# Kernel optimization log

Hardware: AMD Instinct MI355X
Metric: run time of the kernel (lower is better)

## Reference

```python
import jax, jax.numpy as jnp
import numpy as np


def _lstm_encode(x_tbF, W_ih, W_hh, b_ih, b_hh):
    """torch nn.LSTM (single layer), x: [T, B, F]. Returns final (h, c), each [B, H]."""
    H = W_hh.shape[1]
    B = x_tbF.shape[1]
    b = b_ih + b_hh

    def step(carry, xt):
        h, c = carry
        gates = xt @ W_ih.T + h @ W_hh.T + b  # [B, 4H]
        i, f, g, o = jnp.split(gates, 4, axis=-1)
        c = jax.nn.sigmoid(f) * c + jax.nn.sigmoid(i) * jnp.tanh(g)
        h = jax.nn.sigmoid(o) * jnp.tanh(c)
        return (h, c), None

    init = (jnp.zeros((B, H), x_tbF.dtype), jnp.zeros((B, H), x_tbF.dtype))
    (h, c), _ = jax.lax.scan(step, init, x_tbF)
    return h, c


def reference(speed, pos, Ws_ih, Ws_hh, bs_ih, bs_hh, Wp_ih, Wp_hh, bp_ih, bp_hh,
              Wd_ih, Wd_hh, bd_ih, bd_hh, W_fc, b_fc, W_emb, b_emb, seq_len):
    # Encoders consume time-major inputs (module does speed.permute(1,0,2))
    sh, sc = _lstm_encode(jnp.transpose(speed, (1, 0, 2)), Ws_ih, Ws_hh, bs_ih, bs_hh)
    ph, pc = _lstm_encode(jnp.transpose(pos, (1, 0, 2)), Wp_ih, Wp_hh, bp_ih, bp_hh)

    h0 = ph + sh
    c0 = pc + sc
    last_pos0 = pos[:, -1, :]  # [B, 4]
    bd = bd_ih + bd_hh

    def dec_step(carry, _):
        h, c, last_pos = carry
        gates = last_pos @ Wd_ih.T + h @ Wd_hh.T + bd  # [B, 4H]
        i, f, g, o = jnp.split(gates, 4, axis=-1)
        c = jax.nn.sigmoid(f) * c + jax.nn.sigmoid(i) * jnp.tanh(g)
        h = jax.nn.sigmoid(o) * jnp.tanh(c)
        crossing = jax.nn.relu(h @ W_fc.T + b_fc)        # fc_crossing: [B, 2]
        last_pos = jax.nn.relu(crossing @ W_emb.T + b_emb)  # pos_embedding: [B, 4]
        probs = jax.nn.softmax(crossing, axis=1)
        return (h, c, last_pos), probs

    _, probs = jax.lax.scan(dec_step, (h0, c0, last_pos0), None, length=seq_len)
    return jnp.transpose(probs, (1, 0, 2))  # [B, seq_len, 2]


def setup_inputs() -> dict:
    B, T, H, F = 8192, 16, 512, 4
    seq_len = 16
    key = jax.random.key(0)
    ks = jax.random.split(key, 20)
    s = 1.0 / np.sqrt(H)

    def u(k, shape):
        return jax.random.uniform(k, shape, jnp.float32, -s, s)

    return {
        "speed": jax.random.normal(ks[0], (B, T, F), jnp.float32),
        "pos": jax.random.normal(ks[1], (B, T, F), jnp.float32),
        "Ws_ih": u(ks[2], (4 * H, F)), "Ws_hh": u(ks[3], (4 * H, H)),
        "bs_ih": u(ks[4], (4 * H,)), "bs_hh": u(ks[5], (4 * H,)),
        "Wp_ih": u(ks[6], (4 * H, F)), "Wp_hh": u(ks[7], (4 * H, H)),
        "bp_ih": u(ks[8], (4 * H,)), "bp_hh": u(ks[9], (4 * H,)),
        "Wd_ih": u(ks[10], (4 * H, F)), "Wd_hh": u(ks[11], (4 * H, H)),
        "bd_ih": u(ks[12], (4 * H,)), "bd_hh": u(ks[13], (4 * H,)),
        "W_fc": u(ks[14], (2, H)), "b_fc": u(ks[15], (2,)),
        "W_emb": u(ks[16], (4, 2)), "b_emb": u(ks[17], (4,)),
        "seq_len": seq_len,
    }
```

## Files before the change

### kernel.cpp

```cpp
#include <hip/hip_runtime.h>

#define NBLK 256
#define NTHR 512
#define MTILE 32
#define KPADI 592
#define HSTR  528
#define CHB   (9*8*64*16)
#define LSTR  (16*CHB)

typedef __attribute__((ext_vector_type(4))) int int4v;

__device__ inline float ex2(float x){ return __builtin_amdgcn_exp2f(x); }
__device__ inline float rcpf_(float d){ return __builtin_amdgcn_rcpf(d); }
__device__ inline float rcpn(float d){ float r=__builtin_amdgcn_rcpf(d); return r*(2.f-d*r); }
#define LOG2E 1.4426950408889634f
__device__ inline float sigf(float x){ return rcpf_(1.f+ex2(-LOG2E*x)); }
__device__ inline float tanh_(float x){ return 2.f*rcpf_(1.f+ex2(-2.f*LOG2E*x))-1.f; }

__global__ void scale_k(const float* Ws_ih, const float* Ws_hh, const float* bs_ih, const float* bs_hh,
                        const float* Wp_ih, const float* Wp_hh, const float* bp_ih, const float* bp_hh,
                        const float* Wd_ih, const float* Wd_hh, const float* bd_ih, const float* bd_hh,
                        int* smax)
{
    int L = blockIdx.x >> 5;
    int blk = blockIdx.x & 31;
    const float* Wih = L==0 ? Ws_ih : L==1 ? Wp_ih : Wd_ih;
    const float* Whh = L==0 ? Ws_hh : L==1 ? Wp_hh : Wd_hh;
    const float* bih = L==0 ? bs_ih : L==1 ? bp_ih : bd_ih;
    const float* bhh = L==0 ? bs_hh : L==1 ? bp_hh : bd_hh;
    float m = 0.f;
    for (int i = blk*256 + threadIdx.x; i < 2048*512; i += 32*256) m = fmaxf(m, fabsf(Whh[i]));
    for (int i = blk*256 + threadIdx.x; i < 2048*4;   i += 32*256) m = fmaxf(m, fabsf(Wih[i]));
    for (int i = blk*256 + threadIdx.x; i < 2048;     i += 32*256) m = fmaxf(m, 0.5f*fabsf(bih[i]+bhh[i]));
    __shared__ float red[256];
    red[threadIdx.x] = m; __syncthreads();
    for (int s = 128; s; s >>= 1){
        if (threadIdx.x < s) red[threadIdx.x] = fmaxf(red[threadIdx.x], red[threadIdx.x+s]);
        __syncthreads();
    }
    if (threadIdx.x == 0) atomicMax(&smax[L], __float_as_int(red[0]));
}

__global__ void pack_k(const float* Wih, const float* Whh, const float* bih, const float* bhh,
                       const int* smax, int L, unsigned char* dst, float* gsout)
{
    int f4 = blockIdx.x*256 + threadIdx.x;
    if (f4*4 >= LSTR) return;
    float mx = __int_as_float(smax[L]);
    float inv = 127.f / mx;
    if (blockIdx.x==0 && threadIdx.x==0) gsout[L] = mx * (1.f/(127.f*127.f));
    int fb = f4*4;
    int lane=(fb>>4)&63, nt=(fb>>10)&7, t=fb>>13;
    int kt=t%9, chunk=t/9;
    int n = (chunk*8+nt)*16 + (lane&15);
    int ch=n>>7, g=(n>>5)&3, u=n&31;
    int row = g*512 + ch*32 + u;
    int kbase = kt*64 + ((lane>>4)<<4) + (fb&15);
    unsigned out = 0;
    #pragma unroll
    for (int b=0;b<4;++b){
        int k = kbase + b;
        float v = 0.f;
        if (k < 512)      v = Whh[row*512+k];
        else if (k < 528) v = Wih[row*4 + (k&3)];
        else if (k < 530) v = 0.5f*(bih[row]+bhh[row]);
        int q = (int)rintf(v*inv);
        q = q>127?127:(q<-127?-127:q);
        out |= ((unsigned)(q & 255)) << (8*b);
    }
    *(unsigned*)(dst + fb) = out;
}

__global__ __launch_bounds__(NTHR, 1)
void lstm_all(const float* __restrict__ speed, const float* __restrict__ pos,
              const unsigned char* __restrict__ wpack, const float* __restrict__ gsb,
              const float* __restrict__ wfc, const float* __restrict__ bfc,
              const float* __restrict__ wemb, const float* __restrict__ bemb,
              float* __restrict__ out)
{
    __shared__ __align__(16) unsigned char abuf[2][MTILE][KPADI];
    __shared__ __align__(16) unsigned char hsave[MTILE][HSTR];
    __shared__ float csave[MTILE][512];
    __shared__ float smallw[1040];
    __shared__ float partial[NTHR];

    const int tid  = threadIdx.x;
    const int lane = tid & 63;
    const int wv   = tid >> 6;
    const int row0 = blockIdx.x * MTILE;
    const int l15  = lane & 15;
    const int lq   = lane >> 4;
    const int cstag = blockIdx.x & 15;

    const float gs0 = gsb[0], gs1 = gsb[1], gs2 = gsb[2];

    {
        for (int i = tid; i < 2*MTILE*(KPADI/16); i += NTHR) {
            int b = i / (MTILE*(KPADI/16));
            int rmd = i % (MTILE*(KPADI/16));
            int m = rmd / (KPADI/16), c16 = (rmd % (KPADI/16))*16;
            *(int4v*)&abuf[b][m][c16] = (int4v){0,0,0,0};
        }
        for (int i = tid; i < 1024; i += NTHR) smallw[i] = wfc[i];
        if (tid < 2) smallw[1024+tid] = bfc[tid];
        if (tid < 8) smallw[1026+tid] = wemb[tid];
        if (tid < 4) smallw[1034+tid] = bemb[tid];
    }
    __syncthreads();
    if (tid < 64) { int b = tid>>5, m = tid&31; abuf[b][m][528] = 127; abuf[b][m][529] = 127; }
    if (tid < 128) {
        int m = tid>>2, f3 = tid&3;
        float x = speed[((size_t)(row0+m)*16 + 0)*4 + f3];
        int q = (int)rintf(fminf(fmaxf(x*31.75f,-127.f),127.f));
        unsigned char qb = (unsigned char)q;
        abuf[0][m][512+f3]=qb; abuf[0][m][516+f3]=qb; abuf[0][m][520+f3]=qb; abuf[0][m][524+f3]=qb;
    }
    __syncthreads();

    float cc0[16], cc1[16];
    #pragma unroll
    for (int i = 0; i < 16; ++i) { cc0[i]=0.f; cc1[i]=0.f; }

    auto pass = [&](int rb, int wbuf, const unsigned char* wl, int s, float (&cc)[16],
                    float gs, int DUAL, int DEFER, int (&hq)[16]) {
        const int chunk = (2*wv + s + cstag) & 15;
        const unsigned char* bp = wl + (size_t)chunk*CHB + lane*16;
        const unsigned char* ar0 = &abuf[rb][l15][0];
        const unsigned char* ar1 = &abuf[rb][16+l15][0];
        int4v acc[2][8];
        #pragma unroll
        for (int mf=0;mf<2;++mf)
            #pragma unroll
            for (int nt=0;nt<8;++nt) acc[mf][nt] = (int4v){0,0,0,0};
        int4v bA[8], bB[8];
        #pragma unroll
        for (int nt=0;nt<8;++nt) bA[nt] = *(const int4v*)(bp + nt*1024);
        #pragma unroll 1
        for (int kt=0; kt<8; kt+=2){
            const unsigned char* p1 = bp + (kt+1)*8192;
            #pragma unroll
            for (int nt=0;nt<8;++nt) bB[nt] = *(const int4v*)(p1 + nt*1024);
            int4v a0 = *(const int4v*)(ar0 + kt*64 + lq*16);
            int4v a1 = *(const int4v*)(ar1 + kt*64 + lq*16);
            #pragma unroll
            for (int nt=0;nt<8;++nt){
                acc[0][nt] = __builtin_amdgcn_mfma_i32_16x16x64_i8(a0, bA[nt], acc[0][nt], 0,0,0);
                acc[1][nt] = __builtin_amdgcn_mfma_i32_16x16x64_i8(a1, bA[nt], acc[1][nt], 0,0,0);
            }
            const unsigned char* p2 = bp + (kt+2)*8192;
            #pragma unroll
            for (int nt=0;nt<8;++nt) bA[nt] = *(const int4v*)(p2 + nt*1024);
            a0 = *(const int4v*)(ar0 + (kt+1)*64 + lq*16);
            a1 = *(const int4v*)(ar1 + (kt+1)*64 + lq*16);
            #pragma unroll
            for (int nt=0;nt<8;++nt){
                acc[0][nt] = __builtin_amdgcn_mfma_i32_16x16x64_i8(a0, bB[nt], acc[0][nt], 0,0,0);
                acc[1][nt] = __builtin_amdgcn_mfma_i32_16x16x64_i8(a1, bB[nt], acc[1][nt], 0,0,0);
            }
        }
        {
            int4v a0 = *(const int4v*)(ar0 + 8*64 + lq*16);
            int4v a1 = *(const int4v*)(ar1 + 8*64 + lq*16);
            #pragma unroll
            for (int nt=0;nt<8;++nt){
                acc[0][nt] = __builtin_amdgcn_mfma_i32_16x16x64_i8(a0, bA[nt], acc[0][nt], 0,0,0);
                acc[1][nt] = __builtin_amdgcn_mfma_i32_16x16x64_i8(a1, bA[nt], acc[1][nt], 0,0,0);
            }
        }
        if (DUAL) {
            const unsigned char* hr0 = &hsave[l15][0];
            const unsigned char* hr1 = &hsave[16+l15][0];
            #pragma unroll
            for (int nt=0;nt<8;++nt) bA[nt] = *(const int4v*)(bp + nt*1024);
            #pragma unroll 1
            for (int kt=0; kt<8; kt+=2){
                const unsigned char* p1 = bp + (kt+1)*8192;
                #pragma unroll
                for (int nt=0;nt<8;++nt) bB[nt] = *(const int4v*)(p1 + nt*1024);
                int4v a0 = *(const int4v*)(hr0 + kt*64 + lq*16);
                int4v a1 = *(const int4v*)(hr1 + kt*64 + lq*16);
                #pragma unroll
                for (int nt=0;nt<8;++nt){
                    acc[0][nt] = __builtin_amdgcn_mfma_i32_16x16x64_i8(a0, bA[nt], acc[0][nt], 0,0,0);
                    acc[1][nt] = __builtin_amdgcn_mfma_i32_16x16x64_i8(a1, bA[nt], acc[1][nt], 0,0,0);
                }
                const unsigned char* p2 = bp + (kt+2)*8192;
                #pragma unroll
                for (int nt=0;nt<8;++nt) bA[nt] = *(const int4v*)(p2 + nt*1024);
                a0 = *(const int4v*)(hr0 + (kt+1)*64 + lq*16);
                a1 = *(const int4v*)(hr1 + (kt+1)*64 + lq*16);
                #pragma unroll
                for (int nt=0;nt<8;++nt){
                    acc[0][nt] = __builtin_amdgcn_mfma_i32_16x16x64_i8(a0, bB[nt], acc[0][nt], 0,0,0);
                    acc[1][nt] = __builtin_amdgcn_mfma_i32_16x16x64_i8(a1, bB[nt], acc[1][nt], 0,0,0);
                }
            }
        }
        #pragma unroll
        for (int mf=0;mf<2;++mf)
            #pragma unroll
            for (int up=0;up<2;++up)
                #pragma unroll
                for (int r=0;r<4;++r){
                    int idx = (mf*2+up)*4 + r;
                    float gi = (float)acc[mf][0+up][r] * gs;
                    float gf = (float)acc[mf][2+up][r] * gs;
                    float gg = (float)acc[mf][4+up][r] * gs;
                    float go = (float)acc[mf][6+up][r] * gs;
                    float cn = sigf(gf)*cc[idx] + sigf(gi)*tanh_(gg);
                    cc[idx] = cn;
                    float h = sigf(go)*tanh_(cn);
                    int q = (int)rintf(h*127.f);
                    if (DEFER) hq[idx] = q;
                    else abuf[wbuf][mf*16+lq*4+r][chunk*32+up*16+l15] = (unsigned char)q;
                }
    };

    const unsigned char* wsp = wpack;
    const unsigned char* wpp = wpack + (size_t)LSTR;
    const unsigned char* wdp = wpack + 2*(size_t)LSTR;
    int dmy[16];

    #pragma unroll 1
    for (int t=0;t<16;++t){
        int rb=t&1, wbuf=(t+1)&1;
        pass(rb,wbuf,wsp,0,cc0,gs0,0,0,dmy);
        pass(rb,wbuf,wsp,1,cc1,gs0,0,0,dmy);
        if (t<15 && tid<128){
            int m=tid>>2, f3=tid&3;
            float x = speed[((size_t)(row0+m)*16 + t+1)*4 + f3];
            int q = (int)rintf(fminf(fmaxf(x*31.75f,-127.f),127.f));
            unsigned char qb=(unsigned char)q;
            abuf[wbuf][m][512+f3]=qb; abuf[wbuf][m][516+f3]=qb; abuf[wbuf][m][520+f3]=qb; abuf[wbuf][m][524+f3]=qb;
        }
        __syncthreads();
    }
    for (int i=tid; i<MTILE*32; i+=NTHR){
        int m=i>>5, cb=(i&31)*16;
        *(int4v*)&hsave[m][cb] = *(const int4v*)&abuf[0][m][cb];
        *(int4v*)&abuf[0][m][cb] = (int4v){0,0,0,0};
    }
    #pragma unroll
    for (int s2=0;s2<2;++s2)
        #pragma unroll
        for (int mf=0;mf<2;++mf)
            #pragma unroll
            for (int up=0;up<2;++up)
                #pragma unroll
                for (int r=0;r<4;++r){
                    int idx=(mf*2+up)*4+r;
                    int ch=(2*wv+s2+cstag)&15;
                    csave[mf*16+lq*4+r][ch*32+up*16+l15] = s2 ? cc1[idx] : cc0[idx];
                }
    #pragma unroll
    for (int i=0;i<16;++i){ cc0[i]=0.f; cc1[i]=0.f; }
    if (tid < 128) {
        int m = tid>>2, f3 = tid&3;
        float x = pos[((size_t)(row0+m)*16 + 0)*4 + f3];
        int q = (int)rintf(fminf(fmaxf(x*31.75f,-127.f),127.f));
        unsigned char qb = (unsigned char)q;
        abuf[0][m][512+f3]=qb; abuf[0][m][516+f3]=qb; abuf[0][m][520+f3]=qb; abuf[0][m][524+f3]=qb;
    }
    __syncthreads();

    #pragma unroll 1
    for (int t=0;t<16;++t){
        int rb=t&1, wbuf=(t+1)&1;
        pass(rb,wbuf,wpp,0,cc0,gs1,0,0,dmy);
        pass(rb,wbuf,wpp,1,cc1,gs1,0,0,dmy);
        if (t<15 && tid<128){
            int m=tid>>2, f3=tid&3;
            float x = pos[((size_t)(row0+m)*16 + t+1)*4 + f3];
            int q = (int)rintf(fminf(fmaxf(x*31.75f,-127.f),127.f));
            unsigned char qb=(unsigned char)q;
            abuf[wbuf][m][512+f3]=qb; abuf[wbuf][m][516+f3]=qb; abuf[wbuf][m][520+f3]=qb; abuf[wbuf][m][524+f3]=qb;
        }
        __syncthreads();
    }
    if (tid < 128) {
        int m = tid>>2, f3 = tid&3;
        float x = pos[((size_t)(row0+m)*16 + 15)*4 + f3];
        int q = (int)rintf(fminf(fmaxf(x*31.75f,-127.f),127.f));
        unsigned char qb = (unsigned char)q;
        abuf[0][m][512+f3]=qb; abuf[0][m][516+f3]=qb; abuf[0][m][520+f3]=qb; abuf[0][m][524+f3]=qb;
    }
    #pragma unroll
    for (int s2=0;s2<2;++s2)
        #pragma unroll
        for (int mf=0;mf<2;++mf)
            #pragma unroll
            for (int up=0;up<2;++up)
                #pragma unroll
                for (int r=0;r<4;++r){
                    int idx=(mf*2+up)*4+r;
                    int ch=(2*wv+s2+cstag)&15;
                    float v = csave[mf*16+lq*4+r][ch*32+up*16+l15];
                    if (s2) cc1[idx]+=v; else cc0[idx]+=v;
                }
    __syncthreads();

    #pragma unroll 1
    for (int t=0;t<16;++t){
        int hb;
        if (t == 0) {
            int hq0[16], hq1[16];
            pass(0,0,wdp,0,cc0,gs2,1,1,hq0);
            pass(0,0,wdp,1,cc1,gs2,1,1,hq1);
            __syncthreads();
            #pragma unroll
            for (int s2=0;s2<2;++s2)
                #pragma unroll
                for (int mf=0;mf<2;++mf)
                    #pragma unroll
                    for (int up=0;up<2;++up)
                        #pragma unroll
                        for (int r=0;r<4;++r){
                            int idx=(mf*2+up)*4+r;
                            int ch=(2*wv+s2+cstag)&15;
                            int q = s2 ? hq1[idx] : hq0[idx];
                            abuf[0][mf*16+lq*4+r][ch*32+up*16+l15] = (unsigned char)q;
                        }
            hb = 0;
        } else {
            int rb=(t+1)&1, wbuf=t&1;
            pass(rb,wbuf,wdp,0,cc0,gs2,0,0,dmy);
            pass(rb,wbuf,wdp,1,cc1,gs2,0,0,dmy);
            hb = wbuf;
        }
        __syncthreads();
        {
            int r = lane>>1, col = lane&1;
            const unsigned char* hp = &abuf[hb][r][wv*64];
            const float* wp = &smallw[col*512 + wv*64];
            float p = 0.f;
            #pragma unroll
            for (int k4=0;k4<16;++k4){
                int v = *(const int*)(hp + k4*4);
                p += (float)((signed char)(v    )) * wp[k4*4+0];
                p += (float)((signed char)(v>>8 )) * wp[k4*4+1];
                p += (float)((signed char)(v>>16)) * wp[k4*4+2];
                p += (float)((signed char)(v>>24)) * wp[k4*4+3];
            }
            partial[wv*64 + lane] = p;
        }
        __syncthreads();
        if (wv == 0) {
            float p = 0.f;
            #pragma unroll
            for (int i=0;i<8;++i) p += partial[i*64 + lane];
            int r = lane>>1, col = lane&1;
            p = p*(1.f/127.f) + smallw[1024+col];
            float cr = fmaxf(p, 0.f);
            float other = __shfl_xor(cr, 1, 64);
            float mx = fmaxf(cr, other);
            float e0 = ex2(LOG2E*(cr-mx)), e1 = ex2(LOG2E*(other-mx));
            out[((size_t)(row0+r))*32 + t*2 + col] = e0*rcpn(e0+e1);
            float c0v = col ? other : cr;
            float c1v = col ? cr : other;
            #pragma unroll
            for (int q2=0;q2<2;++q2){
                int e = col*2 + q2;
                float lp = fmaxf(c0v*smallw[1026+e*2] + c1v*smallw[1026+e*2+1] + smallw[1034+e], 0.f);
                int qv = (int)rintf(fminf(lp*31.75f, 127.f));
                unsigned char qb = (unsigned char)qv;
                abuf[hb][r][512+e]=qb; abuf[hb][r][516+e]=qb; abuf[hb][r][520+e]=qb; abuf[hb][r][524+e]=qb;
            }
        }
        __syncthreads();
    }
}

extern "C" void kernel_launch(void* const* d_in, const int* in_sizes, int n_in,
                              void* d_out, int out_size, void* d_ws, size_t ws_size,
                              hipStream_t stream)
{
    (void)in_sizes; (void)n_in; (void)out_size; (void)ws_size;
    const float* speed = (const float*)d_in[0];
    const float* pos   = (const float*)d_in[1];
    const float* Ws_ih = (const float*)d_in[2];
    const float* Ws_hh = (const float*)d_in[3];
    const float* bs_ih = (const float*)d_in[4];
    const float* bs_hh = (const float*)d_in[5];
    const float* Wp_ih = (const float*)d_in[6];
    const float* Wp_hh = (const float*)d_in[7];
    const float* bp_ih = (const float*)d_in[8];
    const float* bp_hh = (const float*)d_in[9];
    const float* Wd_ih = (const float*)d_in[10];
    const float* Wd_hh = (const float*)d_in[11];
    const float* bd_ih = (const float*)d_in[12];
    const float* bd_hh = (const float*)d_in[13];
    const float* W_fc  = (const float*)d_in[14];
    const float* b_fc  = (const float*)d_in[15];
    const float* W_emb = (const float*)d_in[16];
    const float* b_emb = (const float*)d_in[17];

    unsigned char* wp8 = (unsigned char*)d_ws;
    int*   smax  = (int*)(wp8 + 3*(size_t)LSTR);
    float* gsout = (float*)(wp8 + 3*(size_t)LSTR + 16);

    scale_k<<<96, 256, 0, stream>>>(Ws_ih,Ws_hh,bs_ih,bs_hh, Wp_ih,Wp_hh,bp_ih,bp_hh,
                                    Wd_ih,Wd_hh,bd_ih,bd_hh, smax);
    int gb = (LSTR/4 + 255) / 256;
    pack_k<<<gb, 256, 0, stream>>>(Ws_ih, Ws_hh, bs_ih, bs_hh, smax, 0, wp8,                  gsout);
    pack_k<<<gb, 256, 0, stream>>>(Wp_ih, Wp_hh, bp_ih, bp_hh, smax, 1, wp8 +   (size_t)LSTR, gsout);
    pack_k<<<gb, 256, 0, stream>>>(Wd_ih, Wd_hh, bd_ih, bd_hh, smax, 2, wp8 + 2*(size_t)LSTR, gsout);
    lstm_all<<<NBLK, NTHR, 0, stream>>>(speed, pos, wp8, gsout,
                                        W_fc, b_fc, W_emb, b_emb, (float*)d_out);
}
```

Baseline: 751.4 us.

## Fuse two chunk passes per step and prefetch weights across passes and timesteps

Replaces the two independent per-chunk passes with a single step2 routine that, while finishing the first chunk's GEMM, loads the second chunk's first weight tile, and at the end of the second chunk prefetches the next timestep's first tile (the weights are the same every step), skipping the initial load on warm steps. The gate-scale multiply is folded into the exponent constants in the epilogue. The input quantization write now comes before the step so the MFMA work and weight loads are not delayed by it. The cost is more live registers, since bA/bB are hoisted out to persist across calls, which may raise register pressure or cause spills.

Result: faster. 727.8 us, median of 2 (-3.1%).

```diff
diff --git a/kernel.cpp b/kernel.cpp
--- a/kernel.cpp
+++ b/kernel.cpp
@@ -121,18 +121,139 @@
     #pragma unroll
     for (int i = 0; i < 16; ++i) { cc0[i]=0.f; cc1[i]=0.f; }
 
-    auto pass = [&](int rb, int wbuf, const unsigned char* wl, int s, float (&cc)[16],
-                    float gs, int DUAL, int DEFER, int (&hq)[16]) {
+    int4v bA[8], bB[8];
+
+    auto epi = [&](int4v (&acc)[2][8], float (&cc)[16], int chunk, int wbuf,
+                   float nK1, float nK2){
+        #pragma unroll
+        for (int mf=0;mf<2;++mf)
+            #pragma unroll
+            for (int up=0;up<2;++up)
+                #pragma unroll
+                for (int r=0;r<4;++r){
+                    int idx = (mf*2+up)*4 + r;
+                    float fi = (float)acc[mf][0+up][r];
+                    float ff = (float)acc[mf][2+up][r];
+                    float fg = (float)acc[mf][4+up][r];
+                    float fo = (float)acc[mf][6+up][r];
+                    float si = rcpf_(1.f+ex2(nK1*fi));
+                    float sf = rcpf_(1.f+ex2(nK1*ff));
+                    float so = rcpf_(1.f+ex2(nK1*fo));
+                    float tg = 2.f*rcpf_(1.f+ex2(nK2*fg)) - 1.f;
+                    float cn = sf*cc[idx] + si*tg;
+                    cc[idx] = cn;
+                    float h = so*tanh_(cn);
+                    int q = (int)rintf(h*127.f);
+                    abuf[wbuf][mf*16+lq*4+r][chunk*32+up*16+l15] = (unsigned char)q;
+                }
+    };
+
+    auto step2 = [&](int rb, int wbuf, const unsigned char* wl,
+                     float (&c0)[16], float (&c1)[16], float gs, int WARM, int PF){
+        const int ch0 = (2*wv + 0 + cstag) & 15;
+        const int ch1 = (2*wv + 1 + cstag) & 15;
+        const unsigned char* bp0 = wl + (size_t)ch0*CHB + lane*16;
+        const unsigned char* bp1 = wl + (size_t)ch1*CHB + lane*16;
+        const unsigned char* ar0 = &abuf[rb][l15][0];
+        const unsigned char* ar1 = &abuf[rb][16+l15][0];
+        const float nK1 = -gs*LOG2E, nK2 = -2.f*gs*LOG2E;
+        int4v acc[2][8];
+        if (!WARM){
+            #pragma unroll
+            for (int nt=0;nt<8;++nt) bA[nt] = *(const int4v*)(bp0 + nt*1024);
+        }
+        #pragma unroll
+        for (int mf=0;mf<2;++mf)
+            #pragma unroll
+            for (int nt=0;nt<8;++nt) acc[mf][nt] = (int4v){0,0,0,0};
+        #pragma unroll 1
+        for (int kt=0; kt<8; kt+=2){
+            const unsigned char* p1 = bp0 + (kt+1)*8192;
+            #pragma unroll
+            for (int nt=0;nt<8;++nt) bB[nt] = *(const int4v*)(p1 + nt*1024);
+            int4v a0 = *(const int4v*)(ar0 + kt*64 + lq*16);
+            int4v a1 = *(const int4v*)(ar1 + kt*64 + lq*16);
+            #pragma unroll
+            for (int nt=0;nt<8;++nt){
+                acc[0][nt] = __builtin_amdgcn_mfma_i32_16x16x64_i8(a0, bA[nt], acc[0][nt], 0,0,0);
+                acc[1][nt] = __builtin_amdgcn_mfma_i32_16x16x64_i8(a1, bA[nt], acc[1][nt], 0,0,0);
+            }
+            const unsigned char* p2 = bp0 + (kt+2)*8192;
+            #pragma unroll
+            for (int nt=0;nt<8;++nt) bA[nt] = *(const int4v*)(p2 + nt*1024);
+            a0 = *(const int4v*)(ar0 + (kt+1)*64 + lq*16);
+            a1 = *(const int4v*)(ar1 + (kt+1)*64 + lq*16);
+            #pragma unroll
+            for (int nt=0;nt<8;++nt){
+                acc[0][nt] = __builtin_amdgcn_mfma_i32_16x16x64_i8(a0, bB[nt], acc[0][nt], 0,0,0);
+                acc[1][nt] = __builtin_amdgcn_mfma_i32_16x16x64_i8(a1, bB[nt], acc[1][nt], 0,0,0);
+            }
+        }
+        #pragma unroll
+        for (int nt=0;nt<8;++nt) bB[nt] = *(const int4v*)(bp1 + nt*1024);
+        {
+            int4v a0 = *(const int4v*)(ar0 + 8*64 + lq*16);
+            int4v a1 = *(const int4v*)(ar1 + 8*64 + lq*16);
+            #pragma unroll
+            for (int nt=0;nt<8;++nt){
+                acc[0][nt] = __builtin_amdgcn_mfma_i32_16x16x64_i8(a0, bA[nt], acc[0][nt], 0,0,0);
+                acc[1][nt] = __builtin_amdgcn_mfma_i32_16x16x64_i8(a1, bA[nt], acc[1][nt], 0,0,0);
+            }
+        }
+        epi(acc, c0, ch0, wbuf, nK1, nK2);
+        #pragma unroll
+        for (int mf=0;mf<2;++mf)
+            #pragma unroll
+            for (int nt=0;nt<8;++nt) acc[mf][nt] = (int4v){0,0,0,0};
+        #pragma unroll 1
+        for (int kt=0; kt<8; kt+=2){
+            const unsigned char* p1 = bp1 + (kt+1)*8192;
+            #pragma unroll
+            for (int nt=0;nt<8;++nt) bA[nt] = *(const int4v*)(p1 + nt*1024);
+            int4v a0 = *(const int4v*)(ar0 + kt*64 + lq*16);
+            int4v a1 = *(const int4v*)(ar1 + kt*64 + lq*16);
+            #pragma unroll
+            for (int nt=0;nt<8;++nt){
+                acc[0][nt] = __builtin_amdgcn_mfma_i32_16x16x64_i8(a0, bB[nt], acc[0][nt], 0,0,0);
+                acc[1][nt] = __builtin_amdgcn_mfma_i32_16x16x64_i8(a1, bB[nt], acc[1][nt], 0,0,0);
+            }
+            const unsigned char* p2 = bp1 + (kt+2)*8192;
+            #pragma unroll
+            for (int nt=0;nt<8;++nt) bB[nt] = *(const int4v*)(p2 + nt*1024);
+            a0 = *(const int4v*)(ar0 + (kt+1)*64 + lq*16);
+            a1 = *(const int4v*)(ar1 + (kt+1)*64 + lq*16);
+            #pragma unroll
+            for (int nt=0;nt<8;++nt){
+                acc[0][nt] = __builtin_amdgcn_mfma_i32_16x16x64_i8(a0, bA[nt], acc[0][nt], 0,0,0);
+                acc[1][nt] = __builtin_amdgcn_mfma_i32_16x16x64_i8(a1, bA[nt], acc[1][nt], 0,0,0);
+            }
+        }
+        if (PF){
+            #pragma unroll
+            for (int nt=0;nt<8;++nt) bA[nt] = *(const int4v*)(bp0 + nt*1024);
+        }
+        {
+            int4v a0 = *(const int4v*)(ar0 + 8*64 + lq*16);
+            int4v a1 = *(const int4v*)(ar1 + 8*64 + lq*16);
+            #pragma unroll
+            for (int nt=0;nt<8;++nt){
+                acc[0][nt] = __builtin_amdgcn_mfma_i32_16x16x64_i8(a0, bB[nt], acc[0][nt], 0,0,0);
+                acc[1][nt] = __builtin_amdgcn_mfma_i32_16x16x64_i8(a1, bB[nt], acc[1][nt], 0,0,0);
+            }
+        }
+        epi(acc, c1, ch1, wbuf, nK1, nK2);
+    };
+
+    auto pass_dual = [&](const unsigned char* wl, int s, float (&cc)[16], float gs, int (&hq)[16]) {
         const int chunk = (2*wv + s + cstag) & 15;
         const unsigned char* bp = wl + (size_t)chunk*CHB + lane*16;
-        const unsigned char* ar0 = &abuf[rb][l15][0];
-        const unsigned char* ar1 = &abuf[rb][16+l15][0];
+        const unsigned char* ar0 = &abuf[0][l15][0];
+        const unsigned char* ar1 = &abuf[0][16+l15][0];
         int4v acc[2][8];
         #pragma unroll
         for (int mf=0;mf<2;++mf)
             #pragma unroll
             for (int nt=0;nt<8;++nt) acc[mf][nt] = (int4v){0,0,0,0};
-        int4v bA[8], bB[8];
         #pragma unroll
         for (int nt=0;nt<8;++nt) bA[nt] = *(const int4v*)(bp + nt*1024);
         #pragma unroll 1
@@ -167,7 +288,7 @@
                 acc[1][nt] = __builtin_amdgcn_mfma_i32_16x16x64_i8(a1, bA[nt], acc[1][nt], 0,0,0);
             }
         }
-        if (DUAL) {
+        {
             const unsigned char* hr0 = &hsave[l15][0];
             const unsigned char* hr1 = &hsave[16+l15][0];
             #pragma unroll
@@ -210,22 +331,17 @@
                     float cn = sigf(gf)*cc[idx] + sigf(gi)*tanh_(gg);
                     cc[idx] = cn;
                     float h = sigf(go)*tanh_(cn);
-                    int q = (int)rintf(h*127.f);
-                    if (DEFER) hq[idx] = q;
-                    else abuf[wbuf][mf*16+lq*4+r][chunk*32+up*16+l15] = (unsigned char)q;
+                    hq[idx] = (int)rintf(h*127.f);
                 }
     };
 
     const unsigned char* wsp = wpack;
     const unsigned char* wpp = wpack + (size_t)LSTR;
     const unsigned char* wdp = wpack + 2*(size_t)LSTR;
-    int dmy[16];
 
     #pragma unroll 1
     for (int t=0;t<16;++t){
         int rb=t&1, wbuf=(t+1)&1;
-        pass(rb,wbuf,wsp,0,cc0,gs0,0,0,dmy);
-        pass(rb,wbuf,wsp,1,cc1,gs0,0,0,dmy);
         if (t<15 && tid<128){
             int m=tid>>2, f3=tid&3;
             float x = speed[((size_t)(row0+m)*16 + t+1)*4 + f3];
@@ -233,6 +349,7 @@
             unsigned char qb=(unsigned char)q;
             abuf[wbuf][m][512+f3]=qb; abuf[wbuf][m][516+f3]=qb; abuf[wbuf][m][520+f3]=qb; abuf[wbuf][m][524+f3]=qb;
         }
+        step2(rb,wbuf,wsp,cc0,cc1,gs0, (t>0), (t<15));
         __syncthreads();
     }
     for (int i=tid; i<MTILE*32; i+=NTHR){
@@ -266,8 +383,6 @@
     #pragma unroll 1
     for (int t=0;t<16;++t){
         int rb=t&1, wbuf=(t+1)&1;
-        pass(rb,wbuf,wpp,0,cc0,gs1,0,0,dmy);
-        pass(rb,wbuf,wpp,1,cc1,gs1,0,0,dmy);
         if (t<15 && tid<128){
             int m=tid>>2, f3=tid&3;
             float x = pos[((size_t)(row0+m)*16 + t+1)*4 + f3];
@@ -275,6 +390,7 @@
             unsigned char qb=(unsigned char)q;
             abuf[wbuf][m][512+f3]=qb; abuf[wbuf][m][516+f3]=qb; abuf[wbuf][m][520+f3]=qb; abuf[wbuf][m][524+f3]=qb;
         }
+        step2(rb,wbuf,wpp,cc0,cc1,gs1, (t>0), (t<15));
         __syncthreads();
     }
     if (tid < 128) {
@@ -304,8 +420,8 @@
         int hb;
         if (t == 0) {
             int hq0[16], hq1[16];
-            pass(0,0,wdp,0,cc0,gs2,1,1,hq0);
-            pass(0,0,wdp,1,cc1,gs2,1,1,hq1);
+            pass_dual(wdp, 0, cc0, gs2, hq0);
+            pass_dual(wdp, 1, cc1, gs2, hq1);
             __syncthreads();
             #pragma unroll
             for (int s2=0;s2<2;++s2)
@@ -323,8 +439,7 @@
             hb = 0;
         } else {
             int rb=(t+1)&1, wbuf=t&1;
-            pass(rb,wbuf,wdp,0,cc0,gs2,0,0,dmy);
-            pass(rb,wbuf,wdp,1,cc1,gs2,0,0,dmy);
+            step2(rb,wbuf,wdp,cc0,cc1,gs2, (t>1), (t<15));
             hb = wbuf;
         }
         __syncthreads();
```

## Double threads per block so each wave owns one hidden chunk

Applied to the files above, without the earlier changes.

Raises block size from 512 to 1024 threads. Each wave now handles a single 32-column hidden chunk instead of two, split into two half-passes (input/forget gates, then gate/output), which cuts per-thread accumulator and weight-register footprint. Gate scale factors are folded into precomputed exponent constants, and the input-row quantization is moved ahead of the pass. The FC reduction is re-split across 16 waves. The cost is higher register pressure per CU from 1024 threads and more waves contending on the same barriers, in exchange for more latency hiding.

New measurement: 995.7 us. 32.5% more time.

```diff
diff --git a/kernel.cpp b/kernel.cpp
--- a/kernel.cpp
+++ b/kernel.cpp
@@ -1,7 +1,7 @@
 #include <hip/hip_runtime.h>
 
 #define NBLK 256
-#define NTHR 512
+#define NTHR 1024
 #define MTILE 32
 #define KPADI 592
 #define HSTR  528
@@ -14,7 +14,6 @@
 __device__ inline float rcpf_(float d){ return __builtin_amdgcn_rcpf(d); }
 __device__ inline float rcpn(float d){ float r=__builtin_amdgcn_rcpf(d); return r*(2.f-d*r); }
 #define LOG2E 1.4426950408889634f
-__device__ inline float sigf(float x){ return rcpf_(1.f+ex2(-LOG2E*x)); }
 __device__ inline float tanh_(float x){ return 2.f*rcpf_(1.f+ex2(-2.f*LOG2E*x))-1.f; }
 
 __global__ void scale_k(const float* Ws_ih, const float* Ws_hh, const float* bs_ih, const float* bs_hh,
@@ -91,6 +90,7 @@
     const int l15  = lane & 15;
     const int lq   = lane >> 4;
     const int cstag = blockIdx.x & 15;
+    const int ch   = (wv + cstag) & 15;
 
     const float gs0 = gsb[0], gs1 = gsb[1], gs2 = gsb[2];
 
@@ -117,82 +117,72 @@
     }
     __syncthreads();
 
-    float cc0[16], cc1[16];
+    float cc[16];
     #pragma unroll
-    for (int i = 0; i < 16; ++i) { cc0[i]=0.f; cc1[i]=0.f; }
-
-    auto pass = [&](int rb, int wbuf, const unsigned char* wl, int s, float (&cc)[16],
-                    float gs, int DUAL, int DEFER, int (&hq)[16]) {
-        const int chunk = (2*wv + s + cstag) & 15;
-        const unsigned char* bp = wl + (size_t)chunk*CHB + lane*16;
+    for (int i = 0; i < 16; ++i) cc[i]=0.f;
+
+    auto pass = [&](int rb, int wbuf, const unsigned char* wl,
+                    float nK1, float nK2, int DUAL, int DEFER, int (&hq)[16]) {
+        const unsigned char* bp0 = wl + (size_t)ch*CHB + lane*16;
+        const unsigned char* bp1 = bp0 + 4*1024;
         const unsigned char* ar0 = &abuf[rb][l15][0];
         const unsigned char* ar1 = &abuf[rb][16+l15][0];
-        int4v acc[2][8];
+        float sI[16];
+        int4v bA[4], bB[4], acc[2][4];
+        #pragma unroll
+        for (int j=0;j<4;++j) bA[j] = *(const int4v*)(bp0 + j*1024);
         #pragma unroll
         for (int mf=0;mf<2;++mf)
             #pragma unroll
-            for (int nt=0;nt<8;++nt) acc[mf][nt] = (int4v){0,0,0,0};
-        int4v bA[8], bB[8];
-        #pragma unroll
-        for (int nt=0;nt<8;++nt) bA[nt] = *(const int4v*)(bp + nt*1024);
+            for (int j=0;j<4;++j) acc[mf][j] = (int4v){0,0,0,0};
         #pragma unroll 1
         for (int kt=0; kt<8; kt+=2){
-            const unsigned char* p1 = bp + (kt+1)*8192;
-            #pragma unroll
-            for (int nt=0;nt<8;++nt) bB[nt] = *(const int4v*)(p1 + nt*1024);
+            const unsigned char* p1 = bp0 + (kt+1)*8192;
+            #pragma unroll
+            for (int j=0;j<4;++j) bB[j] = *(const int4v*)(p1 + j*1024);
             int4v a0 = *(const int4v*)(ar0 + kt*64 + lq*16);
             int4v a1 = *(const int4v*)(ar1 + kt*64 + lq*16);
             #pragma unroll
-            for (int nt=0;nt<8;++nt){
-                acc[0][nt] = __builtin_amdgcn_mfma_i32_16x16x64_i8(a0, bA[nt], acc[0][nt], 0,0,0);
-                acc[1][nt] = __builtin_amdgcn_mfma_i32_16x16x64_i8(a1, bA[nt], acc[1][nt], 0,0,0);
-            }
-            const unsigned char* p2 = bp + (kt+2)*8192;
-            #pragma unroll
-            for (int nt=0;nt<8;++nt) bA[nt] = *(const int4v*)(p2 + nt*1024);
+            for (int j=0;j<4;++j){
+                acc[0][j] = __builtin_amdgcn_mfma_i32_16x16x64_i8(a0, bA[j], acc[0][j], 0,0,0);
+                acc[1][j] = __builtin_amdgcn_mfma_i32_16x16x64_i8(a1, bA[j], acc[1][j], 0,0,0);
+            }
+            const unsigned char* p2 = bp0 + (kt+2)*8192;
+            #pragma unroll
+            for (int j=0;j<4;++j) bA[j] = *(const int4v*)(p2 + j*1024);
             a0 = *(const int4v*)(ar0 + (kt+1)*64 + lq*16);
             a1 = *(const int4v*)(ar1 + (kt+1)*64 + lq*16);
             #pragma unroll
-            for (int nt=0;nt<8;++nt){
-                acc[0][nt] = __builtin_amdgcn_mfma_i32_16x16x64_i8(a0, bB[nt], acc[0][nt], 0,0,0);
-                acc[1][nt] = __builtin_amdgcn_mfma_i32_16x16x64_i8(a1, bB[nt], acc[1][nt], 0,0,0);
-            }
-        }
+            for (int j=0;j<4;++j){
+                acc[0][j] = __builtin_amdgcn_mfma_i32_16x16x64_i8(a0, bB[j], acc[0][j], 0,0,0);
+                acc[1][j] = __builtin_amdgcn_mfma_i32_16x16x64_i8(a1, bB[j], acc[1][j], 0,0,0);
+            }
+        }
+        #pragma unroll
+        for (int j=0;j<4;++j) bB[j] = *(const int4v*)(bp1 + j*1024);
         {
             int4v a0 = *(const int4v*)(ar0 + 8*64 + lq*16);
             int4v a1 = *(const int4v*)(ar1 + 8*64 + lq*16);
             #pragma unroll
-            for (int nt=0;nt<8;++nt){
-                acc[0][nt] = __builtin_amdgcn_mfma_i32_16x16x64_i8(a0, bA[nt], acc[0][nt], 0,0,0);
-                acc[1][nt] = __builtin_amdgcn_mfma_i32_16x16x64_i8(a1, bA[nt], acc[1][nt], 0,0,0);
+            for (int j=0;j<4;++j){
+                acc[0][j] = __builtin_amdgcn_mfma_i32_16x16x64_i8(a0, bA[j], acc[0][j], 0,0,0);
+                acc[1][j] = __builtin_amdgcn_mfma_i32_16x16x64_i8(a1, bA[j], acc[1][j], 0,0,0);
             }
         }
         if (DUAL) {
             const unsigned char* hr0 = &hsave[l15][0];
             const unsigned char* hr1 = &hsave[16+l15][0];
-            #pragma unroll
-            for (int nt=0;nt<8;++nt) bA[nt] = *(const int4v*)(bp + nt*1024);
             #pragma unroll 1
-            for (int kt=0; kt<8; kt+=2){
-                const unsigned char* p1 = bp + (kt+1)*8192;
-                #pragma unroll
-                for (int nt=0;nt<8;++nt) bB[nt] = *(const int4v*)(p1 + nt*1024);
+            for (int kt=0; kt<8; ++kt){
+                const unsigned char* p = bp0 + kt*8192;
+                #pragma unroll
+                for (int j=0;j<4;++j) bA[j] = *(const int4v*)(p + j*1024);
                 int4v a0 = *(const int4v*)(hr0 + kt*64 + lq*16);
                 int4v a1 = *(const int4v*)(hr1 + kt*64 + lq*16);
                 #pragma unroll
-                for (int nt=0;nt<8;++nt){
-                    acc[0][nt] = __builtin_amdgcn_mfma_i32_16x16x64_i8(a0, bA[nt], acc[0][nt], 0,0,0);
-                    acc[1][nt] = __builtin_amdgcn_mfma_i32_16x16x64_i8(a1, bA[nt], acc[1][nt], 0,0,0);
-                }
-                const unsigned char* p2 = bp + (kt+2)*8192;
-                #pragma unroll
-                for (int nt=0;nt<8;++nt) bA[nt] = *(const int4v*)(p2 + nt*1024);
-                a0 = *(const int4v*)(hr0 + (kt+1)*64 + lq*16);
-                a1 = *(const int4v*)(hr1 + (kt+1)*64 + lq*16);
-                #pragma unroll
-                for (int nt=0;nt<8;++nt){
-                    acc[0][nt] = __builtin_amdgcn_mfma_i32_16x16x64_i8(a0, bB[nt], acc[0][nt], 0,0,0);
-                    acc[1][nt] = __builtin_amdgcn_mfma_i32_16x16x64_i8(a1, bB[nt], acc[1][nt], 0,0,0);
+                for (int j=0;j<4;++j){
+                    acc[0][j] = __builtin_amdgcn_mfma_i32_16x16x64_i8(a0, bA[j], acc[0][j], 0,0,0);
+                    acc[1][j] = __builtin_amdgcn_mfma_i32_16x16x64_i8(a1, bA[j], acc[1][j], 0,0,0);
                 }
             }
         }
@@ -203,16 +193,77 @@
                 #pragma unroll
                 for (int r=0;r<4;++r){
                     int idx = (mf*2+up)*4 + r;
-                    float gi = (float)acc[mf][0+up][r] * gs;
-                    float gf = (float)acc[mf][2+up][r] * gs;
-                    float gg = (float)acc[mf][4+up][r] * gs;
-                    float go = (float)acc[mf][6+up][r] * gs;
-                    float cn = sigf(gf)*cc[idx] + sigf(gi)*tanh_(gg);
+                    sI[idx] = rcpf_(1.f+ex2(nK1*(float)acc[mf][0+up][r]));
+                    cc[idx] = rcpf_(1.f+ex2(nK1*(float)acc[mf][2+up][r])) * cc[idx];
+                }
+        #pragma unroll
+        for (int mf=0;mf<2;++mf)
+            #pragma unroll
+            for (int j=0;j<4;++j) acc[mf][j] = (int4v){0,0,0,0};
+        #pragma unroll 1
+        for (int kt=0; kt<8; kt+=2){
+            const unsigned char* p1 = bp1 + (kt+1)*8192;
+            #pragma unroll
+            for (int j=0;j<4;++j) bA[j] = *(const int4v*)(p1 + j*1024);
+            int4v a0 = *(const int4v*)(ar0 + kt*64 + lq*16);
+            int4v a1 = *(const int4v*)(ar1 + kt*64 + lq*16);
+            #pragma unroll
+            for (int j=0;j<4;++j){
+                acc[0][j] = __builtin_amdgcn_mfma_i32_16x16x64_i8(a0, bB[j], acc[0][j], 0,0,0);
+                acc[1][j] = __builtin_amdgcn_mfma_i32_16x16x64_i8(a1, bB[j], acc[1][j], 0,0,0);
+            }
+            const unsigned char* p2 = bp1 + (kt+2)*8192;
+            #pragma unroll
+            for (int j=0;j<4;++j) bB[j] = *(const int4v*)(p2 + j*1024);
+            a0 = *(const int4v*)(ar0 + (kt+1)*64 + lq*16);
+            a1 = *(const int4v*)(ar1 + (kt+1)*64 + lq*16);
+            #pragma unroll
+            for (int j=0;j<4;++j){
+                acc[0][j] = __builtin_amdgcn_mfma_i32_16x16x64_i8(a0, bA[j], acc[0][j], 0,0,0);
+                acc[1][j] = __builtin_amdgcn_mfma_i32_16x16x64_i8(a1, bA[j], acc[1][j], 0,0,0);
+            }
+        }
+        {
+            int4v a0 = *(const int4v*)(ar0 + 8*64 + lq*16);
+            int4v a1 = *(const int4v*)(ar1 + 8*64 + lq*16);
+            #pragma unroll
+            for (int j=0;j<4;++j){
+                acc[0][j] = __builtin_amdgcn_mfma_i32_16x16x64_i8(a0, bB[j], acc[0][j], 0,0,0);
+                acc[1][j] = __builtin_amdgcn_mfma_i32_16x16x64_i8(a1, bB[j], acc[1][j], 0,0,0);
+            }
+        }
+        if (DUAL) {
+            const unsigned char* hr0 = &hsave[l15][0];
+            const unsigned char* hr1 = &hsave[16+l15][0];
+            #pragma unroll 1
+            for (int kt=0; kt<8; ++kt){
+                const unsigned char* p = bp1 + kt*8192;
+                #pragma unroll
+                for (int j=0;j<4;++j) bA[j] = *(const int4v*)(p + j*1024);
+                int4v a0 = *(const int4v*)(hr0 + kt*64 + lq*16);
+                int4v a1 = *(const int4v*)(hr1 + kt*64 + lq*16);
+                #pragma unroll
+                for (int j=0;j<4;++j){
+                    acc[0][j] = __builtin_amdgcn_mfma_i32_16x16x64_i8(a0, bA[j], acc[0][j], 0,0,0);
+                    acc[1][j] = __builtin_amdgcn_mfma_i32_16x16x64_i8(a1, bA[j], acc[1][j], 0,0,0);
+                }
+            }
+        }
+        #pragma unroll
+        for (int mf=0;mf<2;++mf)
+            #pragma unroll
+            for (int up=0;up<2;++up)
+                #pragma unroll
+                for (int r=0;r<4;++r){
+                    int idx = (mf*2+up)*4 + r;
+                    float tg = 2.f*rcpf_(1.f+ex2(nK2*(float)acc[mf][0+up][r])) - 1.f;
+                    float so = rcpf_(1.f+ex2(nK1*(float)acc[mf][2+up][r]));
+                    float cn = cc[idx] + sI[idx]*tg;
                     cc[idx] = cn;
-                    float h = sigf(go)*tanh_(cn);
+                    float h = so*tanh_(cn);
                     int q = (int)rintf(h*127.f);
                     if (DEFER) hq[idx] = q;
-                    else abuf[wbuf][mf*16+lq*4+r][chunk*32+up*16+l15] = (unsigned char)q;
+                    else abuf[wbuf][mf*16+lq*4+r][ch*32+up*16+l15] = (unsigned char)q;
                 }
     };
 
@@ -221,19 +272,21 @@
     const unsigned char* wdp = wpack + 2*(size_t)LSTR;
     int dmy[16];
 
-    #pragma unroll 1
-    for (int t=0;t<16;++t){
-        int rb=t&1, wbuf=(t+1)&1;
-        pass(rb,wbuf,wsp,0,cc0,gs0,0,0,dmy);
-        pass(rb,wbuf,wsp,1,cc1,gs0,0,0,dmy);
-        if (t<15 && tid<128){
-            int m=tid>>2, f3=tid&3;
-            float x = speed[((size_t)(row0+m)*16 + t+1)*4 + f3];
-            int q = (int)rintf(fminf(fmaxf(x*31.75f,-127.f),127.f));
-            unsigned char qb=(unsigned char)q;
-            abuf[wbuf][m][512+f3]=qb; abuf[wbuf][m][516+f3]=qb; abuf[wbuf][m][520+f3]=qb; abuf[wbuf][m][524+f3]=qb;
-        }
-        __syncthreads();
+    {
+        const float nK1 = -gs0*LOG2E, nK2 = -2.f*gs0*LOG2E;
+        #pragma unroll 1
+        for (int t=0;t<16;++t){
+            int rb=t&1, wbuf=(t+1)&1;
+            if (t<15 && tid<128){
+                int m=tid>>2, f3=tid&3;
+                float x = speed[((size_t)(row0+m)*16 + t+1)*4 + f3];
+                int q = (int)rintf(fminf(fmaxf(x*31.75f,-127.f),127.f));
+                unsigned char qb=(unsigned char)q;
+                abuf[wbuf][m][512+f3]=qb; abuf[wbuf][m][516+f3]=qb; abuf[wbuf][m][520+f3]=qb; abuf[wbuf][m][524+f3]=qb;
+            }
+            pass(rb,wbuf,wsp,nK1,nK2,0,0,dmy);
+            __syncthreads();
+        }
     }
     for (int i=tid; i<MTILE*32; i+=NTHR){
         int m=i>>5, cb=(i&31)*16;
@@ -241,19 +294,16 @@
         *(int4v*)&abuf[0][m][cb] = (int4v){0,0,0,0};
     }
     #pragma unroll
-    for (int s2=0;s2<2;++s2)
-        #pragma unroll
-        for (int mf=0;mf<2;++mf)
-            #pragma unroll
-            for (int up=0;up<2;++up)
-                #pragma unroll
-                for (int r=0;r<4;++r){
-                    int idx=(mf*2+up)*4+r;
-                    int ch=(2*wv+s2+cstag)&15;
-                    csave[mf*16+lq*4+r][ch*32+up*16+l15] = s2 ? cc1[idx] : cc0[idx];
-                }
+    for (int mf=0;mf<2;++mf)
+        #pragma unroll
+        for (int up=0;up<2;++up)
+            #pragma unroll
+            for (int r=0;r<4;++r){
+                int idx=(mf*2+up)*4+r;
+                csave[mf*16+lq*4+r][ch*32+up*16+l15] = cc[idx];
+            }
     #pragma unroll
-    for (int i=0;i<16;++i){ cc0[i]=0.f; cc1[i]=0.f; }
+    for (int i=0;i<16;++i) cc[i]=0.f;
     if (tid < 128) {
         int m = tid>>2, f3 = tid&3;
         float x = pos[((size_t)(row0+m)*16 + 0)*4 + f3];
@@ -263,19 +313,21 @@
     }
     __syncthreads();
 
-    #pragma unroll 1
-    for (int t=0;t<16;++t){
-        int rb=t&1, wbuf=(t+1)&1;
-        pass(rb,wbuf,wpp,0,cc0,gs1,0,0,dmy);
-        pass(rb,wbuf,wpp,1,cc1,gs1,0,0,dmy);
-        if (t<15 && tid<128){
-            int m=tid>>2, f3=tid&3;
-            float x = pos[((size_t)(row0+m)*16 + t+1)*4 + f3];
-            int q = (int)rintf(fminf(fmaxf(x*31.75f,-127.f),127.f));
-            unsigned char qb=(unsigned char)q;
-            abuf[wbuf][m][512+f3]=qb; abuf[wbuf][m][516+f3]=qb; abuf[wbuf][m][520+f3]=qb; abuf[wbuf][m][524+f3]=qb;
-        }
-        __syncthreads();
+    {
+        const float nK1 = -gs1*LOG2E, nK2 = -2.f*gs1*LOG2E;
+        #pragma unroll 1
+        for (int t=0;t<16;++t){
+            int rb=t&1, wbuf=(t+1)&1;
+            if (t<15 && tid<128){
+                int m=tid>>2, f3=tid&3;
+                float x = pos[((size_t)(row0+m)*16 + t+1)*4 + f3];
+                int q = (int)rintf(fminf(fmaxf(x*31.75f,-127.f),127.f));
+                unsigned char qb=(unsigned char)q;
+                abuf[wbuf][m][512+f3]=qb; abuf[wbuf][m][516+f3]=qb; abuf[wbuf][m][520+f3]=qb; abuf[wbuf][m][524+f3]=qb;
+            }
+            pass(rb,wbuf,wpp,nK1,nK2,0,0,dmy);
+            __syncthreads();
+        }
     }
     if (tid < 128) {
         int m = tid>>2, f3 = tid&3;
@@ -285,30 +337,25 @@
         abuf[0][m][512+f3]=qb; abuf[0][m][516+f3]=qb; abuf[0][m][520+f3]=qb; abuf[0][m][524+f3]=qb;
     }
     #pragma unroll
-    for (int s2=0;s2<2;++s2)
-        #pragma unroll
-        for (int mf=0;mf<2;++mf)
-            #pragma unroll
-            for (int up=0;up<2;++up)
-                #pragma unroll
-                for (int r=0;r<4;++r){
-                    int idx=(mf*2+up)*4+r;
-                    int ch=(2*wv+s2+cstag)&15;
-                    float v = csave[mf*16+lq*4+r][ch*32+up*16+l15];
-                    if (s2) cc1[idx]+=v; else cc0[idx]+=v;
-                }
+    for (int mf=0;mf<2;++mf)
+        #pragma unroll
+        for (int up=0;up<2;++up)
+            #pragma unroll
+            for (int r=0;r<4;++r){
+                int idx=(mf*2+up)*4+r;
+                cc[idx] += csave[mf*16+lq*4+r][ch*32+up*16+l15];
+            }
     __syncthreads();
 
-    #pragma unroll 1
-    for (int t=0;t<16;++t){
-        int hb;
-        if (t == 0) {
-            int hq0[16], hq1[16];
-            pass(0,0,wdp,0,cc0,gs2,1,1,hq0);
-            pass(0,0,wdp,1,cc1,gs2,1,1,hq1);
-            __syncthreads();
-            #pragma unroll
-            for (int s2=0;s2<2;++s2)
+    {
+        const float nK1 = -gs2*LOG2E, nK2 = -2.f*gs2*LOG2E;
+        #pragma unroll 1
+        for (int t=0;t<16;++t){
+            int hb;
+            if (t == 0) {
+                int hq[16];
+                pass(0,0,wdp,nK1,nK2,1,1,hq);
+                __syncthreads();
                 #pragma unroll
                 for (int mf=0;mf<2;++mf)
                     #pragma unroll
@@ -316,57 +363,55 @@
                         #pragma unroll
                         for (int r=0;r<4;++r){
                             int idx=(mf*2+up)*4+r;
-                            int ch=(2*wv+s2+cstag)&15;
-                            int q = s2 ? hq1[idx] : hq0[idx];
-                            abuf[0][mf*16+lq*4+r][ch*32+up*16+l15] = (unsigned char)q;
+                            abuf[0][mf*16+lq*4+r][ch*32+up*16+l15] = (unsigned char)hq[idx];
                         }
-            hb = 0;
-        } else {
-            int rb=(t+1)&1, wbuf=t&1;
-            pass(rb,wbuf,wdp,0,cc0,gs2,0,0,dmy);
-            pass(rb,wbuf,wdp,1,cc1,gs2,0,0,dmy);
-            hb = wbuf;
-        }
-        __syncthreads();
-        {
-            int r = lane>>1, col = lane&1;
-            const unsigned char* hp = &abuf[hb][r][wv*64];
-            const float* wp = &smallw[col*512 + wv*64];
-            float p = 0.f;
-            #pragma unroll
-            for (int k4=0;k4<16;++k4){
-                int v = *(const int*)(hp + k4*4);
-                p += (float)((signed char)(v    )) * wp[k4*4+0];
-                p += (float)((signed char)(v>>8 )) * wp[k4*4+1];
-                p += (float)((signed char)(v>>16)) * wp[k4*4+2];
-                p += (float)((signed char)(v>>24)) * wp[k4*4+3];
-            }
-            partial[wv*64 + lane] = p;
-        }
-        __syncthreads();
-        if (wv == 0) {
-            float p = 0.f;
-            #pragma unroll
-            for (int i=0;i<8;++i) p += partial[i*64 + lane];
-            int r = lane>>1, col = lane&1;
-            p = p*(1.f/127.f) + smallw[1024+col];
-            float cr = fmaxf(p, 0.f);
-            float other = __shfl_xor(cr, 1, 64);
-            float mx = fmaxf(cr, other);
-            float e0 = ex2(LOG2E*(cr-mx)), e1 = ex2(LOG2E*(other-mx));
-            out[((size_t)(row0+r))*32 + t*2 + col] = e0*rcpn(e0+e1);
-            float c0v = col ? other : cr;
-            float c1v = col ? cr : other;
-            #pragma unroll
-            for (int q2=0;q2<2;++q2){
-                int e = col*2 + q2;
-                float lp = fmaxf(c0v*smallw[1026+e*2] + c1v*smallw[1026+e*2+1] + smallw[1034+e], 0.f);
-                int qv = (int)rintf(fminf(lp*31.75f, 127.f));
-                unsigned char qb = (unsigned char)qv;
-                abuf[hb][r][512+e]=qb; abuf[hb][r][516+e]=qb; abuf[hb][r][520+e]=qb; abuf[hb][r][524+e]=qb;
-            }
-        }
-        __syncthreads();
+                hb = 0;
+            } else {
+                int rb=(t+1)&1, wbuf=t&1;
+                pass(rb,wbuf,wdp,nK1,nK2,0,0,dmy);
+                hb = wbuf;
+            }
+            __syncthreads();
+            {
+                int r = lane>>1, col = lane&1;
+                const unsigned char* hp = &abuf[hb][r][wv*32];
+                const float* wp = &smallw[col*512 + wv*32];
+                float p = 0.f;
+                #pragma unroll
+                for (int k4=0;k4<8;++k4){
+                    int v = *(const int*)(hp + k4*4);
+                    p += (float)((signed char)(v    )) * wp[k4*4+0];
+                    p += (float)((signed char)(v>>8 )) * wp[k4*4+1];
+                    p += (float)((signed char)(v>>16)) * wp[k4*4+2];
+                    p += (float)((signed char)(v>>24)) * wp[k4*4+3];
+                }
+                partial[wv*64 + lane] = p;
+            }
+            __syncthreads();
+            if (wv == 0) {
+                float p = 0.f;
+                #pragma unroll
+                for (int i=0;i<16;++i) p += partial[i*64 + lane];
+                int r = lane>>1, col = lane&1;
+                p = p*(1.f/127.f) + smallw[1024+col];
+                float cr = fmaxf(p, 0.f);
+                float other = __shfl_xor(cr, 1, 64);
+                float mx = fmaxf(cr, other);
+                float e0 = ex2(LOG2E*(cr-mx)), e1 = ex2(LOG2E*(other-mx));
+                out[((size_t)(row0+r))*32 + t*2 + col] = e0*rcpn(e0+e1);
+                float c0v = col ? other : cr;
+                float c1v = col ? cr : other;
+                #pragma unroll
+                for (int q2=0;q2<2;++q2){
+                    int e = col*2 + q2;
+                    float lp = fmaxf(c0v*smallw[1026+e*2] + c1v*smallw[1026+e*2+1] + smallw[1034+e], 0.f);
+                    int qv = (int)rintf(fminf(lp*31.75f, 127.f));
+                    unsigned char qb = (unsigned char)qv;
+                    abuf[hb][r][512+e]=qb; abuf[hb][r][516+e]=qb; abuf[hb][r][520+e]=qb; abuf[hb][r][524+e]=qb;
+                }
+            }
+            __syncthreads();
+        }
     }
 }
 
```
